# Optimization experiments

Hardware: AMD Instinct MI355X
Metric: run time of the kernel (lower is better)

The kernel has to match this reference:

```python
import jax, jax.numpy as jnp
import numpy as np

LOSS_WEIGHT = 1.0


def _norm_gram(feat):
    # feat: [B, C, H, W] -> normalized channel gram [B, C, C]
    B, C, H, W = feat.shape
    F = feat.reshape(B, C, H * W)                      # [B, C, HW]
    gram = jnp.einsum('bcn,bdn->bcd', F, F)            # [B, C, C]
    n = jnp.sqrt(jnp.sum(F * F, axis=2))               # [B, C] per-channel L2 norm
    norm_M = n[:, :, None] * n[:, None, :]             # [B, C, C]
    return gram / norm_M


def setup_inputs() -> dict:
    key = jax.random.key(0)
    k1, k2 = jax.random.split(key)
    det = jax.random.normal(k1, (8, 512, 128, 128), dtype=jnp.float32)
    sr = jax.random.normal(k2, (8, 512, 128, 128), dtype=jnp.float32)
    return {"det": det, "sr": sr}


def reference(det, sr):
    sm_det = _norm_gram(det)
    sm_sr = _norm_gram(sr)
    # use_l2=True -> MSELoss (mean reduction); weighted_loss with weight=None,
    # reduction='mean' on a scalar is identity; then * loss_weight.
    loss = jnp.mean((sm_det - sm_sr) ** 2)
    return loss * LOSS_WEIGHT
```

## Files before the change

kernel.cpp:

```cpp
#include <hip/hip_runtime.h>
#include <hip/hip_bf16.h>

#define C_CH 512
#define HW 16384
#define NB 8
#define TILE 128
#define BK 32
#define NTB 4
#define NTILES 10
#define KSPLIT 8
#define KCHUNK (HW / KSPLIT)
#define KSTEPS (KCHUNK / BK)
#define NGRAM 16
#define CC (C_CH * C_CH)
#define LOSS_BLOCKS 1024
#define GRID (NGRAM * KSPLIT * NTILES)
#define PANEL_V8 (TILE * BK / 8)

typedef float f32x4 __attribute__((ext_vector_type(4)));
typedef float f32x8 __attribute__((ext_vector_type(8)));
typedef __bf16 bf16x8 __attribute__((ext_vector_type(8)));

__device__ __forceinline__ int slot_of(int R, int c) {
    return (R >> 1) * 8 + ((((R & 1) << 2) + c) ^ ((R >> 1) & 7));
}

__global__ __launch_bounds__(256, 3) void gram_kernel(const float* __restrict__ det,
                                                      const float* __restrict__ sr,
                                                      float* __restrict__ gram) {
    const int lbid = ((int)blockIdx.x & 7) * (GRID / 8) + ((int)blockIdx.x >> 3);
    const int t = lbid % NTILES;
    const int gk = lbid / NTILES;
    const int ks = gk & (KSPLIT - 1);
    const int g = gk >> 3;
    const int tensor = g >> 3, b = g & 7;

    int ti = 0, tt = t;
    while (tt >= NTB - ti) { tt -= NTB - ti; ++ti; }
    const int tj = ti + tt;
    const bool diag = (ti == tj);

    const float* F = (tensor ? sr : det) + (size_t)b * C_CH * HW;
    const float* Abase = F + (size_t)(ti * TILE) * HW + ks * KCHUNK;
    const float* Bbase = F + (size_t)(tj * TILE) * HW + ks * KCHUNK;

    __shared__ bf16x8 lds[4 * PANEL_V8];

    const int tid = threadIdx.x;
    const int lane = tid & 63;
    const int wid = tid >> 6;
    const int wr = wid >> 1, wc = wid & 1;

    int goff[2], lslot[2];
    #pragma unroll
    for (int q = 0; q < 2; ++q) {
        int c = q * 256 + tid;
        int r = c >> 2, ch = c & 3;
        goff[q] = r * HW + ch * 8;
        lslot[q] = slot_of(r, ch);
    }

    f32x8 va[2], vb[2];
    auto LOAD = [&](int kt) {
        const int ko = kt * BK;
        #pragma unroll
        for (int q = 0; q < 2; ++q) va[q] = *(const f32x8*)(Abase + goff[q] + ko);
        if (!diag) {
            #pragma unroll
            for (int q = 0; q < 2; ++q) vb[q] = *(const f32x8*)(Bbase + goff[q] + ko);
        }
    };
    auto WRITE = [&](int buf) {
        bf16x8* As = lds + buf * 2 * PANEL_V8;
        #pragma unroll
        for (int q = 0; q < 2; ++q) {
            bf16x8 h;
            #pragma unroll
            for (int i = 0; i < 8; ++i) h[i] = (__bf16)va[q][i];
            As[lslot[q]] = h;
        }
        if (!diag) {
            bf16x8* Bs = As + PANEL_V8;
            #pragma unroll
            for (int q = 0; q < 2; ++q) {
                bf16x8 h;
                #pragma unroll
                for (int i = 0; i < 8; ++i) h[i] = (__bf16)vb[q][i];
                Bs[lslot[q]] = h;
            }
        }
    };

    f32x4 acc[4][4] = {};
    const int kg = lane >> 4;
    const int l15 = lane & 15;
    auto COMPUTE = [&](int buf) {
        const bf16x8* As = lds + buf * 2 * PANEL_V8;
        const bf16x8* Bs = diag ? As : As + PANEL_V8;
        bf16x8 af[4], bfr[4];
        #pragma unroll
        for (int m = 0; m < 4; ++m) {
            int R = wr * 64 + m * 16 + l15;
            af[m] = As[slot_of(R, kg)];
        }
        #pragma unroll
        for (int n = 0; n < 4; ++n) {
            int R = wc * 64 + n * 16 + l15;
            bfr[n] = Bs[slot_of(R, kg)];
        }
        #pragma unroll
        for (int m = 0; m < 4; ++m)
            #pragma unroll
            for (int n = 0; n < 4; ++n)
                if (!diag || (wc * 64 + n * 16 + 16 > wr * 64 + m * 16))
                    acc[m][n] = __builtin_amdgcn_mfma_f32_16x16x32_bf16(af[m], bfr[n], acc[m][n], 0, 0, 0);
    };

    LOAD(0);
    WRITE(0);
    __syncthreads();
    int cur = 0;
    #pragma unroll 1
    for (int kt = 0; kt < KSTEPS; ++kt) {
        if (kt + 1 < KSTEPS) LOAD(kt + 1);
        COMPUTE(cur);
        if (kt + 1 < KSTEPS) WRITE(cur ^ 1);
        __syncthreads();
        cur ^= 1;
    }

    float* gout = gram + (size_t)g * CC;
    const int rb = ti * TILE + wr * 64 + (kg << 2);
    const int cb = tj * TILE + wc * 64 + l15;
    #pragma unroll
    for (int m = 0; m < 4; ++m)
        #pragma unroll
        for (int n = 0; n < 4; ++n) {
            if (diag && (wc * 64 + n * 16 + 16 <= wr * 64 + m * 16)) continue;
            #pragma unroll
            for (int j = 0; j < 4; ++j)
                atomicAdd(&gout[(size_t)(rb + m * 16 + j) * C_CH + cb + n * 16], acc[m][n][j]);
        }
}

__global__ void norm_kernel(const float* __restrict__ gram, float* __restrict__ invn) {
    const int g = blockIdx.x, c = threadIdx.x;
    float v = gram[(size_t)g * CC + (size_t)c * C_CH + c];
    invn[g * C_CH + c] = 1.0f / sqrtf(v);
}

__global__ __launch_bounds__(256) void loss_kernel(const float* __restrict__ gram,
                                                   const float* __restrict__ invn,
                                                   float* __restrict__ partials) {
    const int tid = threadIdx.x;
    float s = 0.f;
    for (int idx = blockIdx.x * 256 + tid; idx < NB * CC; idx += LOSS_BLOCKS * 256) {
        int b = idx >> 18;
        int c = (idx >> 9) & 511;
        int d = idx & 511;
        int cc = c, dd = d;
        if (dd < cc) { int tmp = cc; cc = dd; dd = tmp; }
        float gd = gram[(size_t)b * CC + (size_t)cc * C_CH + dd];
        float gs = gram[(size_t)(8 + b) * CC + (size_t)cc * C_CH + dd];
        float sd = gd * invn[b * C_CH + c] * invn[b * C_CH + d];
        float ss = gs * invn[(8 + b) * C_CH + c] * invn[(8 + b) * C_CH + d];
        float diff = sd - ss;
        s += diff * diff;
    }
    #pragma unroll
    for (int off = 32; off > 0; off >>= 1) s += __shfl_down(s, off, 64);
    __shared__ float red[4];
    if ((tid & 63) == 0) red[tid >> 6] = s;
    __syncthreads();
    if (tid == 0) partials[blockIdx.x] = red[0] + red[1] + red[2] + red[3];
}

__global__ void final_kernel(const float* __restrict__ partials, float* __restrict__ out) {
    const int tid = threadIdx.x;
    float s = 0.f;
    for (int i = tid; i < LOSS_BLOCKS; i += 256) s += partials[i];
    #pragma unroll
    for (int off = 32; off > 0; off >>= 1) s += __shfl_down(s, off, 64);
    __shared__ float red[4];
    if ((tid & 63) == 0) red[tid >> 6] = s;
    __syncthreads();
    if (tid == 0) out[0] = (red[0] + red[1] + red[2] + red[3]) * (1.0f / (float)(NB * (size_t)CC));
}

extern "C" void kernel_launch(void* const* d_in, const int* in_sizes, int n_in,
                              void* d_out, int out_size, void* d_ws, size_t ws_size,
                              hipStream_t stream) {
    const float* det = (const float*)d_in[0];
    const float* sr  = (const float*)d_in[1];
    float* gram     = (float*)d_ws;
    float* invn     = gram + (size_t)NGRAM * CC;
    float* partials = invn + NGRAM * C_CH;
    float* out      = (float*)d_out;

    hipMemsetAsync(gram, 0, (size_t)NGRAM * CC * sizeof(float), stream);
    gram_kernel<<<GRID, 256, 0, stream>>>(det, sr, gram);
    norm_kernel<<<NGRAM, C_CH, 0, stream>>>(gram, invn);
    loss_kernel<<<LOSS_BLOCKS, 256, 0, stream>>>(gram, invn, partials);
    final_kernel<<<1, 256, 0, stream>>>(partials, out);
}
```

Baseline: 257.5 us.

## Deepen gram kernel prefetch to two register stages and relax occupancy bound

Measured after the change: 253.5 us. Within noise of the previous version (-1.6%).

```diff
diff --git a/kernel.cpp b/kernel.cpp
--- a/kernel.cpp
+++ b/kernel.cpp
@@ -25,7 +25,7 @@
     return (R >> 1) * 8 + ((((R & 1) << 2) + c) ^ ((R >> 1) & 7));
 }
 
-__global__ __launch_bounds__(256, 3) void gram_kernel(const float* __restrict__ det,
+__global__ __launch_bounds__(256, 2) void gram_kernel(const float* __restrict__ det,
                                                       const float* __restrict__ sr,
                                                       float* __restrict__ gram) {
     const int lbid = ((int)blockIdx.x & 7) * (GRID / 8) + ((int)blockIdx.x >> 3);
@@ -60,23 +60,32 @@
         lslot[q] = slot_of(r, ch);
     }
 
-    f32x8 va[2], vb[2];
-    auto LOAD = [&](int kt) {
+    f32x8 a0[2], b0[2], a1[2], b1[2];
+    auto LOAD0 = [&](int kt) {
         const int ko = kt * BK;
         #pragma unroll
-        for (int q = 0; q < 2; ++q) va[q] = *(const f32x8*)(Abase + goff[q] + ko);
-        if (!diag) {
-            #pragma unroll
-            for (int q = 0; q < 2; ++q) vb[q] = *(const f32x8*)(Bbase + goff[q] + ko);
-        }
-    };
-    auto WRITE = [&](int buf) {
-        bf16x8* As = lds + buf * 2 * PANEL_V8;
+        for (int q = 0; q < 2; ++q) a0[q] = *(const f32x8*)(Abase + goff[q] + ko);
+        if (!diag) {
+            #pragma unroll
+            for (int q = 0; q < 2; ++q) b0[q] = *(const f32x8*)(Bbase + goff[q] + ko);
+        }
+    };
+    auto LOAD1 = [&](int kt) {
+        const int ko = kt * BK;
+        #pragma unroll
+        for (int q = 0; q < 2; ++q) a1[q] = *(const f32x8*)(Abase + goff[q] + ko);
+        if (!diag) {
+            #pragma unroll
+            for (int q = 0; q < 2; ++q) b1[q] = *(const f32x8*)(Bbase + goff[q] + ko);
+        }
+    };
+    auto WRITE0 = [&]() {
+        bf16x8* As = lds;
         #pragma unroll
         for (int q = 0; q < 2; ++q) {
             bf16x8 h;
             #pragma unroll
-            for (int i = 0; i < 8; ++i) h[i] = (__bf16)va[q][i];
+            for (int i = 0; i < 8; ++i) h[i] = (__bf16)a0[q][i];
             As[lslot[q]] = h;
         }
         if (!diag) {
@@ -85,7 +94,27 @@
             for (int q = 0; q < 2; ++q) {
                 bf16x8 h;
                 #pragma unroll
-                for (int i = 0; i < 8; ++i) h[i] = (__bf16)vb[q][i];
+                for (int i = 0; i < 8; ++i) h[i] = (__bf16)b0[q][i];
+                Bs[lslot[q]] = h;
+            }
+        }
+    };
+    auto WRITE1 = [&]() {
+        bf16x8* As = lds + 2 * PANEL_V8;
+        #pragma unroll
+        for (int q = 0; q < 2; ++q) {
+            bf16x8 h;
+            #pragma unroll
+            for (int i = 0; i < 8; ++i) h[i] = (__bf16)a1[q][i];
+            As[lslot[q]] = h;
+        }
+        if (!diag) {
+            bf16x8* Bs = As + PANEL_V8;
+            #pragma unroll
+            for (int q = 0; q < 2; ++q) {
+                bf16x8 h;
+                #pragma unroll
+                for (int i = 0; i < 8; ++i) h[i] = (__bf16)b1[q][i];
                 Bs[lslot[q]] = h;
             }
         }
@@ -94,8 +123,7 @@
     f32x4 acc[4][4] = {};
     const int kg = lane >> 4;
     const int l15 = lane & 15;
-    auto COMPUTE = [&](int buf) {
-        const bf16x8* As = lds + buf * 2 * PANEL_V8;
+    auto COMPUTE = [&](const bf16x8* As) {
         const bf16x8* Bs = diag ? As : As + PANEL_V8;
         bf16x8 af[4], bfr[4];
         #pragma unroll
@@ -116,17 +144,21 @@
                     acc[m][n] = __builtin_amdgcn_mfma_f32_16x16x32_bf16(af[m], bfr[n], acc[m][n], 0, 0, 0);
     };
 
-    LOAD(0);
-    WRITE(0);
+    LOAD0(0);
+    WRITE0();
+    LOAD1(1);
     __syncthreads();
-    int cur = 0;
+
     #pragma unroll 1
-    for (int kt = 0; kt < KSTEPS; ++kt) {
-        if (kt + 1 < KSTEPS) LOAD(kt + 1);
-        COMPUTE(cur);
-        if (kt + 1 < KSTEPS) WRITE(cur ^ 1);
+    for (int kt = 0; kt < KSTEPS; kt += 2) {
+        if (kt + 2 < KSTEPS) LOAD0(kt + 2);
+        COMPUTE(lds);
+        WRITE1();
         __syncthreads();
-        cur ^= 1;
+        if (kt + 3 < KSTEPS) LOAD1(kt + 3);
+        COMPUTE(lds + 2 * PANEL_V8);
+        if (kt + 2 < KSTEPS) WRITE0();
+        __syncthreads();
     }
 
     float* gout = gram + (size_t)g * CC;
```

## Enlarge gram tiles to 256 with 8-wave blocks and lighter barriers

Applied to the files above, without the earlier changes.

Result: slower. 433.7 us (+68.4%).

```diff
diff --git a/kernel.cpp b/kernel.cpp
--- a/kernel.cpp
+++ b/kernel.cpp
@@ -4,41 +4,45 @@
 #define C_CH 512
 #define HW 16384
 #define NB 8
-#define TILE 128
+#define TILE 256
 #define BK 32
-#define NTB 4
-#define NTILES 10
-#define KSPLIT 8
+#define NTILES 3
+#define KSPLIT 16
 #define KCHUNK (HW / KSPLIT)
 #define KSTEPS (KCHUNK / BK)
 #define NGRAM 16
 #define CC (C_CH * C_CH)
 #define LOSS_BLOCKS 1024
-#define GRID (NGRAM * KSPLIT * NTILES)
+#define GRID (NGRAM * NTILES * KSPLIT)
 #define PANEL_V8 (TILE * BK / 8)
 
 typedef float f32x4 __attribute__((ext_vector_type(4)));
 typedef float f32x8 __attribute__((ext_vector_type(8)));
 typedef __bf16 bf16x8 __attribute__((ext_vector_type(8)));
 
+#define BAR()                                                       \
+    do {                                                            \
+        asm volatile("s_waitcnt lgkmcnt(0)" ::: "memory");          \
+        __builtin_amdgcn_s_barrier();                               \
+    } while (0)
+
 __device__ __forceinline__ int slot_of(int R, int c) {
     return (R >> 1) * 8 + ((((R & 1) << 2) + c) ^ ((R >> 1) & 7));
 }
 
-__global__ __launch_bounds__(256, 3) void gram_kernel(const float* __restrict__ det,
-                                                      const float* __restrict__ sr,
-                                                      float* __restrict__ gram) {
-    const int lbid = ((int)blockIdx.x & 7) * (GRID / 8) + ((int)blockIdx.x >> 3);
-    const int t = lbid % NTILES;
-    const int gk = lbid / NTILES;
-    const int ks = gk & (KSPLIT - 1);
-    const int g = gk >> 3;
+__global__ __launch_bounds__(512) void gram_kernel(const float* __restrict__ det,
+                                                   const float* __restrict__ sr,
+                                                   float* __restrict__ gram) {
+    const int bid = (int)blockIdx.x;
+    const int idx = bid >> 3;
+    const int g = (bid & 7) * 2 + idx / 48;
+    const int rem = idx % 48;
+    const int ks = rem / 3;
+    const int t = rem % 3;
     const int tensor = g >> 3, b = g & 7;
-
-    int ti = 0, tt = t;
-    while (tt >= NTB - ti) { tt -= NTB - ti; ++ti; }
-    const int tj = ti + tt;
-    const bool diag = (ti == tj);
+    const int ti = (t == 2) ? 1 : 0;
+    const int tj = (t == 0) ? 0 : 1;
+    const bool diag = (t != 1);
 
     const float* F = (tensor ? sr : det) + (size_t)b * C_CH * HW;
     const float* Abase = F + (size_t)(ti * TILE) * HW + ks * KCHUNK;
@@ -49,12 +53,12 @@
     const int tid = threadIdx.x;
     const int lane = tid & 63;
     const int wid = tid >> 6;
-    const int wr = wid >> 1, wc = wid & 1;
+    const int wr = wid >> 2, wc = wid & 3;
 
     int goff[2], lslot[2];
     #pragma unroll
     for (int q = 0; q < 2; ++q) {
-        int c = q * 256 + tid;
+        int c = q * 512 + tid;
         int r = c >> 2, ch = c & 3;
         goff[q] = r * HW + ch * 8;
         lslot[q] = slot_of(r, ch);
@@ -91,16 +95,15 @@
         }
     };
 
-    f32x4 acc[4][4] = {};
+    f32x4 acc[8][4] = {};
     const int kg = lane >> 4;
     const int l15 = lane & 15;
-    auto COMPUTE = [&](int buf) {
-        const bf16x8* As = lds + buf * 2 * PANEL_V8;
+    auto COMPUTE = [&](const bf16x8* As) {
         const bf16x8* Bs = diag ? As : As + PANEL_V8;
-        bf16x8 af[4], bfr[4];
-        #pragma unroll
-        for (int m = 0; m < 4; ++m) {
-            int R = wr * 64 + m * 16 + l15;
+        bf16x8 af[8], bfr[4];
+        #pragma unroll
+        for (int m = 0; m < 8; ++m) {
+            int R = wr * 128 + m * 16 + l15;
             af[m] = As[slot_of(R, kg)];
         }
         #pragma unroll
@@ -108,35 +111,38 @@
             int R = wc * 64 + n * 16 + l15;
             bfr[n] = Bs[slot_of(R, kg)];
         }
-        #pragma unroll
-        for (int m = 0; m < 4; ++m)
+        __builtin_amdgcn_s_setprio(1);
+        #pragma unroll
+        for (int m = 0; m < 8; ++m)
             #pragma unroll
             for (int n = 0; n < 4; ++n)
-                if (!diag || (wc * 64 + n * 16 + 16 > wr * 64 + m * 16))
+                if (!diag || (wc * 64 + n * 16 + 16 > wr * 128 + m * 16))
                     acc[m][n] = __builtin_amdgcn_mfma_f32_16x16x32_bf16(af[m], bfr[n], acc[m][n], 0, 0, 0);
+        __builtin_amdgcn_s_setprio(0);
     };
 
     LOAD(0);
     WRITE(0);
-    __syncthreads();
+    BAR();
     int cur = 0;
+
     #pragma unroll 1
     for (int kt = 0; kt < KSTEPS; ++kt) {
         if (kt + 1 < KSTEPS) LOAD(kt + 1);
-        COMPUTE(cur);
+        COMPUTE(lds + cur * 2 * PANEL_V8);
         if (kt + 1 < KSTEPS) WRITE(cur ^ 1);
-        __syncthreads();
+        BAR();
         cur ^= 1;
     }
 
     float* gout = gram + (size_t)g * CC;
-    const int rb = ti * TILE + wr * 64 + (kg << 2);
+    const int rb = ti * TILE + wr * 128 + (kg << 2);
     const int cb = tj * TILE + wc * 64 + l15;
     #pragma unroll
-    for (int m = 0; m < 4; ++m)
+    for (int m = 0; m < 8; ++m)
         #pragma unroll
         for (int n = 0; n < 4; ++n) {
-            if (diag && (wc * 64 + n * 16 + 16 <= wr * 64 + m * 16)) continue;
+            if (diag && (wc * 64 + n * 16 + 16 <= wr * 128 + m * 16)) continue;
             #pragma unroll
             for (int j = 0; j < 4; ++j)
                 atomicAdd(&gout[(size_t)(rb + m * 16 + j) * C_CH + cb + n * 16], acc[m][n][j]);
@@ -198,7 +204,7 @@
     float* out      = (float*)d_out;
 
     hipMemsetAsync(gram, 0, (size_t)NGRAM * CC * sizeof(float), stream);
-    gram_kernel<<<GRID, 256, 0, stream>>>(det, sr, gram);
+    gram_kernel<<<GRID, 512, 0, stream>>>(det, sr, gram);
     norm_kernel<<<NGRAM, C_CH, 0, stream>>>(gram, invn);
     loss_kernel<<<LOSS_BLOCKS, 256, 0, stream>>>(gram, invn, partials);
     final_kernel<<<1, 256, 0, stream>>>(partials, out);
```

## Stage fp32 panels via global_load_lds and convert to bf16 at fragment read

Applied to the files above, without the earlier changes.

New measurement: 270.2 us. 4.9% more time.

```diff
diff --git a/kernel.cpp b/kernel.cpp
--- a/kernel.cpp
+++ b/kernel.cpp
@@ -15,20 +15,21 @@
 #define CC (C_CH * C_CH)
 #define LOSS_BLOCKS 1024
 #define GRID (NGRAM * KSPLIT * NTILES)
-#define PANEL_V8 (TILE * BK / 8)
+#define PANEL_SLOTS (TILE * 8)
 
 typedef float f32x4 __attribute__((ext_vector_type(4)));
-typedef float f32x8 __attribute__((ext_vector_type(8)));
 typedef __bf16 bf16x8 __attribute__((ext_vector_type(8)));
 
-__device__ __forceinline__ int slot_of(int R, int c) {
-    return (R >> 1) * 8 + ((((R & 1) << 2) + c) ^ ((R >> 1) & 7));
-}
+#define GLOAD_LDS16(gsrc, ldst)                                                 \
+    __builtin_amdgcn_global_load_lds(                                           \
+        (const __attribute__((address_space(1))) void*)(gsrc),                  \
+        (__attribute__((address_space(3))) void*)(ldst), 16, 0, 0)
 
-__global__ __launch_bounds__(256, 3) void gram_kernel(const float* __restrict__ det,
+__global__ __launch_bounds__(256, 2) void gram_kernel(const float* __restrict__ det,
                                                       const float* __restrict__ sr,
                                                       float* __restrict__ gram) {
-    const int lbid = ((int)blockIdx.x & 7) * (GRID / 8) + ((int)blockIdx.x >> 3);
+    const int bid = (int)blockIdx.x;
+    const int lbid = (bid & 7) * (GRID / 8) + (bid >> 3);
     const int t = lbid % NTILES;
     const int gk = lbid / NTILES;
     const int ks = gk & (KSPLIT - 1);
@@ -44,70 +45,54 @@
     const float* Abase = F + (size_t)(ti * TILE) * HW + ks * KCHUNK;
     const float* Bbase = F + (size_t)(tj * TILE) * HW + ks * KCHUNK;
 
-    __shared__ bf16x8 lds[4 * PANEL_V8];
+    __shared__ f32x4 lds[2][2][PANEL_SLOTS];
 
     const int tid = threadIdx.x;
     const int lane = tid & 63;
     const int wid = tid >> 6;
     const int wr = wid >> 1, wc = wid & 1;
+    const int kg = lane >> 4;
+    const int l15 = lane & 15;
 
-    int goff[2], lslot[2];
-    #pragma unroll
-    for (int q = 0; q < 2; ++q) {
-        int c = q * 256 + tid;
-        int r = c >> 2, ch = c & 3;
-        goff[q] = r * HW + ch * 8;
-        lslot[q] = slot_of(r, ch);
-    }
-
-    f32x8 va[2], vb[2];
-    auto LOAD = [&](int kt) {
-        const int ko = kt * BK;
+    auto STAGE = [&](int buf, int kt) {
+        const float* sA = Abase + kt * BK;
         #pragma unroll
-        for (int q = 0; q < 2; ++q) va[q] = *(const f32x8*)(Abase + goff[q] + ko);
-        if (!diag) {
-            #pragma unroll
-            for (int q = 0; q < 2; ++q) vb[q] = *(const f32x8*)(Bbase + goff[q] + ko);
-        }
-    };
-    auto WRITE = [&](int buf) {
-        bf16x8* As = lds + buf * 2 * PANEL_V8;
-        #pragma unroll
-        for (int q = 0; q < 2; ++q) {
-            bf16x8 h;
-            #pragma unroll
-            for (int i = 0; i < 8; ++i) h[i] = (__bf16)va[q][i];
-            As[lslot[q]] = h;
+        for (int q = 0; q < 4; ++q) {
+            int f = q * 256 + tid;
+            int R = f >> 3, s = f & 7;
+            int c = s ^ (R & 7);
+            GLOAD_LDS16(sA + (size_t)R * HW + c * 4, &lds[buf][0][f]);
         }
         if (!diag) {
-            bf16x8* Bs = As + PANEL_V8;
+            const float* sB = Bbase + kt * BK;
             #pragma unroll
-            for (int q = 0; q < 2; ++q) {
-                bf16x8 h;
-                #pragma unroll
-                for (int i = 0; i < 8; ++i) h[i] = (__bf16)vb[q][i];
-                Bs[lslot[q]] = h;
+            for (int q = 0; q < 4; ++q) {
+                int f = q * 256 + tid;
+                int R = f >> 3, s = f & 7;
+                int c = s ^ (R & 7);
+                GLOAD_LDS16(sB + (size_t)R * HW + c * 4, &lds[buf][1][f]);
             }
         }
     };
 
+    auto rdfrag = [&](const f32x4* P, int R) {
+        f32x4 lo = P[R * 8 + ((2 * kg) ^ (R & 7))];
+        f32x4 hi = P[R * 8 + ((2 * kg + 1) ^ (R & 7))];
+        bf16x8 h;
+        #pragma unroll
+        for (int i = 0; i < 4; ++i) { h[i] = (__bf16)lo[i]; h[4 + i] = (__bf16)hi[i]; }
+        return h;
+    };
+
     f32x4 acc[4][4] = {};
-    const int kg = lane >> 4;
-    const int l15 = lane & 15;
     auto COMPUTE = [&](int buf) {
-        const bf16x8* As = lds + buf * 2 * PANEL_V8;
-        const bf16x8* Bs = diag ? As : As + PANEL_V8;
+        const f32x4* As = &lds[buf][0][0];
+        const f32x4* Bs = diag ? As : &lds[buf][1][0];
         bf16x8 af[4], bfr[4];
         #pragma unroll
-        for (int m = 0; m < 4; ++m) {
-            int R = wr * 64 + m * 16 + l15;
-            af[m] = As[slot_of(R, kg)];
-        }
+        for (int m = 0; m < 4; ++m) af[m] = rdfrag(As, wr * 64 + m * 16 + l15);
         #pragma unroll
-        for (int n = 0; n < 4; ++n) {
-            int R = wc * 64 + n * 16 + l15;
-            bfr[n] = Bs[slot_of(R, kg)];
-        }
+        for (int n = 0; n < 4; ++n) bfr[n] = rdfrag(Bs, wc * 64 + n * 16 + l15);
         #pragma unroll
         for (int m = 0; m < 4; ++m)
             #pragma unroll
@@ -116,17 +101,22 @@
                     acc[m][n] = __builtin_amdgcn_mfma_f32_16x16x32_bf16(af[m], bfr[n], acc[m][n], 0, 0, 0);
     };
 
-    LOAD(0);
-    WRITE(0);
-    __syncthreads();
-    int cur = 0;
+    STAGE(0, 0);
     #pragma unroll 1
     for (int kt = 0; kt < KSTEPS; ++kt) {
-        if (kt + 1 < KSTEPS) LOAD(kt + 1);
-        COMPUTE(cur);
-        if (kt + 1 < KSTEPS) WRITE(cur ^ 1);
-        __syncthreads();
-        cur ^= 1;
+        if (kt + 1 < KSTEPS) {
+            STAGE((kt + 1) & 1, kt + 1);
+            if (diag) asm volatile("s_waitcnt vmcnt(4)" ::: "memory");
+            else      asm volatile("s_waitcnt vmcnt(8)" ::: "memory");
+        } else {
+            asm volatile("s_waitcnt vmcnt(0)" ::: "memory");
+        }
+        __builtin_amdgcn_s_barrier();
+        asm volatile("" ::: "memory");
+        COMPUTE(kt & 1);
+        asm volatile("s_waitcnt lgkmcnt(0)" ::: "memory");
+        __builtin_amdgcn_s_barrier();
+        asm volatile("" ::: "memory");
     }
 
     float* gout = gram + (size_t)g * CC;
```
